# Optimization experiments

Measured on AMD Instinct MI355X. Metric: run time of the kernel, lower is better.

The kernel has to match this reference:

```python
import jax, jax.numpy as jnp
import numpy as np

B = 16384          # batch
F = 64             # number of feature columns (tables)
L = 10             # pooled lookups per feature (bag size)
E = 16             # embedding dim
V = 1_000_000      # hashed vocab size (shared table)
D = F * E          # concat width = 1024
EPS = 1e-5


def setup_inputs() -> dict:
    key = jax.random.key(0)
    ks = jax.random.split(key, 9)
    idx = jax.random.randint(ks[0], (B, F, L), 0, V, dtype=jnp.int64)
    # NormalTensorInitializer(var=0.01) -> std 0.1
    emb = jax.random.normal(ks[1], (V, E), dtype=jnp.float32) * 0.1
    W1 = jax.random.normal(ks[2], (D, 1024), dtype=jnp.float32) / np.sqrt(D).astype(np.float32)
    b1 = jnp.zeros((1024,), jnp.float32)
    W2 = jax.random.normal(ks[3], (1024, 512), dtype=jnp.float32) / np.sqrt(1024).astype(np.float32)
    b2 = jnp.zeros((512,), jnp.float32)
    W3 = jax.random.normal(ks[4], (512, 1), dtype=jnp.float32) / np.sqrt(512).astype(np.float32)
    b3 = jnp.zeros((1,), jnp.float32)
    return {"idx": idx, "emb": emb, "W1": W1, "b1": b1,
            "W2": W2, "b2": b2, "W3": W3, "b3": b3}


def reference(idx, emb, W1, b1, W2, b2, W3, b3):
    # EmbeddingSumConcat: gather [B,F,L,E], sum-pool over bag dim, concat features
    pooled = jnp.take(emb, idx, axis=0).sum(axis=2)          # [B, F, E]
    x = pooled.reshape(B, D)                                  # [B, F*E]
    # ms.nn.Normalization: per-feature batch standardization
    mu = x.mean(axis=0, keepdims=True)
    var = x.var(axis=0, keepdims=True)
    x = (x - mu) * jax.lax.rsqrt(var + EPS)
    # Dense tower 1024 -> 1024 -> 512 -> 1, sigmoid
    h = jax.nn.relu(x @ W1 + b1)
    h = jax.nn.relu(h @ W2 + b2)
    out = jax.nn.sigmoid(h @ W3 + b3)                         # [B, 1]
    return out
```

## Files before the change

### kernel.cpp

```cpp
#include <hip/hip_runtime.h>
#include <hip/hip_bf16.h>
#include <math.h>

typedef __attribute__((ext_vector_type(8))) short  short8;
typedef __attribute__((ext_vector_type(4))) float  f32x4;
typedef __attribute__((ext_vector_type(4))) unsigned short u16x4;
typedef __attribute__((ext_vector_type(8))) unsigned short u16x8;

#define BATCH 16384
#define NF    64
#define BAGL  10
#define ED    16
#define DW    1024
#define VOCAB 1000000

static __device__ __forceinline__ unsigned short f2bf(float f) {
    unsigned int u = __builtin_bit_cast(unsigned int, f);
    unsigned int r = (u + 0x7fffu + ((u >> 16) & 1u)) >> 16;
    return (unsigned short)r;
}
static __device__ __forceinline__ float bf2f(unsigned short h) {
    unsigned int u = ((unsigned int)h) << 16;
    return __builtin_bit_cast(float, u);
}

__global__ __launch_bounds__(256) void pool_kernel(const int* __restrict__ idx,
                                                   const float* __restrict__ emb,
                                                   unsigned short* __restrict__ xb) {
    const int gid = blockIdx.x * 256 + threadIdx.x;
    const int bag = gid >> 2;
    const int q   = gid & 3;
    const int* ip = idx + (long long)bag * BAGL;
    const unsigned qb = (unsigned)(q << 4);

    unsigned o0 = ((unsigned)ip[0] << 6) + qb, o1 = ((unsigned)ip[1] << 6) + qb,
             o2 = ((unsigned)ip[2] << 6) + qb, o3 = ((unsigned)ip[3] << 6) + qb,
             o4 = ((unsigned)ip[4] << 6) + qb, o5 = ((unsigned)ip[5] << 6) + qb,
             o6 = ((unsigned)ip[6] << 6) + qb, o7 = ((unsigned)ip[7] << 6) + qb,
             o8 = ((unsigned)ip[8] << 6) + qb, o9 = ((unsigned)ip[9] << 6) + qb;

    f32x4 e0, e1, e2, e3, e4, e5, e6, e7, e8, e9;
#define GLD(e, o) asm volatile("global_load_dwordx4 %0, %1, %2" \
                               : "=v"(e) : "v"(o), "s"(emb))
    GLD(e0, o0); GLD(e1, o1); GLD(e2, o2); GLD(e3, o3); GLD(e4, o4);
    GLD(e5, o5); GLD(e6, o6); GLD(e7, o7); GLD(e8, o8); GLD(e9, o9);
#undef GLD
    asm volatile("s_waitcnt vmcnt(0)" ::: "memory");
    __builtin_amdgcn_sched_barrier(0);

    f32x4 s01 = e0 + e1, s23 = e2 + e3, s45 = e4 + e5, s67 = e6 + e7, s89 = e8 + e9;
    f32x4 acc = ((s01 + s23) + (s45 + s67)) + s89;

    u16x4 o;
#pragma unroll
    for (int j = 0; j < 4; ++j) o[j] = f2bf(acc[j]);
    *(u16x4*)(xb + (((long long)bag) << 4) + (q << 2)) = o;
}

__global__ __launch_bounds__(256) void stats_kernel(const unsigned short* __restrict__ xb,
                                                    float* __restrict__ ssum,
                                                    float* __restrict__ ssq) {
    const int t = threadIdx.x;
    const long long r0 = (long long)blockIdx.x * 64;
    float s[4] = {0, 0, 0, 0}, q[4] = {0, 0, 0, 0};
    for (int r = 0; r < 64; ++r) {
        const u16x4 v = *(const u16x4*)(xb + (r0 + r) * DW + t * 4);
#pragma unroll
        for (int j = 0; j < 4; ++j) { float f = bf2f(v[j]); s[j] += f; q[j] += f * f; }
    }
#pragma unroll
    for (int j = 0; j < 4; ++j) {
        atomicAdd(&ssum[t * 4 + j], s[j]);
        atomicAdd(&ssq [t * 4 + j], q[j]);
    }
}

static __device__ __forceinline__ float rsig_of(const float* ssum, const float* ssq, int c) {
    const float m = ssum[c] * (1.0f / (float)BATCH);
    const float v = ssq[c] * (1.0f / (float)BATCH) - m * m;
    return rsqrtf(v + 1e-5f);
}

__global__ __launch_bounds__(256) void prep_weights(const float* __restrict__ W1,
                                                    const float* __restrict__ W2,
                                                    const float* __restrict__ ssum,
                                                    const float* __restrict__ ssq,
                                                    unsigned short* __restrict__ w1t,
                                                    unsigned short* __restrict__ w2t) {
    const int z = blockIdx.z;
    const int bx = blockIdx.x, by = blockIdx.y;
    if (z == 1 && bx >= 16) return;
    __shared__ float tile[32][33];
    const int tx = threadIdx.x & 31, ty = threadIdx.x >> 5;
    const float* src = z ? W2 : W1;
    unsigned short* dst = z ? w2t : w1t;
    const int C = z ? 512 : 1024;
#pragma unroll
    for (int i = 0; i < 4; ++i) {
        const int r = by * 32 + ty + i * 8, c = bx * 32 + tx;
        float v = src[(long long)r * C + c];
        if (!z) v *= rsig_of(ssum, ssq, r);
        tile[ty + i * 8][tx] = v;
    }
    __syncthreads();
#pragma unroll
    for (int i = 0; i < 4; ++i) {
        const int oc = bx * 32 + ty + i * 8;
        dst[(long long)oc * 1024 + by * 32 + tx] = f2bf(tile[tx][ty + i * 8]);
    }
}

__global__ __launch_bounds__(256) void b1fold_kernel(const float* __restrict__ W1,
                                                     const float* __restrict__ ssum,
                                                     const float* __restrict__ ssq,
                                                     float* __restrict__ b1n) {
    __shared__ float mu_s[128];
    const int n = blockIdx.x * 256 + threadIdx.x;
    const int k0 = blockIdx.y * 128;
    if (threadIdx.x < 128) {
        const int k = k0 + threadIdx.x;
        mu_s[threadIdx.x] = ssum[k] * (1.0f / (float)BATCH) * rsig_of(ssum, ssq, k);
    }
    __syncthreads();
    float acc = 0.f;
#pragma unroll 4
    for (int k = 0; k < 128; ++k)
        acc += mu_s[k] * W1[(long long)(k0 + k) * 1024 + n];
    atomicAdd(&b1n[n], -acc);
}

__global__ __launch_bounds__(512, 2) void gemm1_256(const unsigned short* __restrict__ A,
                                                    const unsigned short* __restrict__ Bt,
                                                    const float* __restrict__ bias,
                                                    const float* __restrict__ bias2,
                                                    unsigned short* __restrict__ C,
                                                    int M, int N, int K) {
    __shared__ __align__(16) unsigned short As[2][256 * 64];
    __shared__ __align__(16) unsigned short Bs[2][256 * 64];
    const int tid = threadIdx.x;
    const int w = tid >> 6, l = tid & 63;
    const int wr = w >> 2, wc = w & 3;
    const int l15 = l & 15, l4 = l >> 4;
    const int blk = blockIdx.x, xcd = blk & 7, jj = blk >> 3;
    const int bm = xcd * 8 + (jj >> 2), bn = jj & 3;

    f32x4 acc[8][4] = {};
    const long long a_base = (long long)bm * 256 * K;
    const long long b_base = (long long)bn * 256 * K;
    const int NT = K >> 6;

#define G1_STAGE(buf, kt)                                                       \
  {                                                                             \
    const int k0s = (kt) * 64;                                                  \
    _Pragma("unroll")                                                           \
    for (int g = 0; g < 4; ++g) {                                               \
      const int cid = g * 512 + tid;                                            \
      const int rr = cid >> 3, pos = cid & 7;                                   \
      const int csrc = (pos ^ (rr & 7)) << 3;                                   \
      __builtin_amdgcn_global_load_lds(                                         \
        (const __attribute__((address_space(1))) void*)(A + a_base + (long long)rr * K + k0s + csrc), \
        (__attribute__((address_space(3))) void*)(&As[buf][cid * 8]), 16, 0, 0);\
      __builtin_amdgcn_global_load_lds(                                         \
        (const __attribute__((address_space(1))) void*)(Bt + b_base + (long long)rr * K + k0s + csrc), \
        (__attribute__((address_space(3))) void*)(&Bs[buf][cid * 8]), 16, 0, 0);\
    }                                                                           \
  }

    G1_STAGE(0, 0)
    G1_STAGE(1, 1)
    asm volatile("s_waitcnt vmcnt(8)" ::: "memory");
    __builtin_amdgcn_sched_barrier(0);
    __builtin_amdgcn_s_barrier();

    for (int t = 0; t < NT; ++t) {
        const unsigned short* Ap = As[t & 1];
        const unsigned short* Bp = Bs[t & 1];
        short8 a[8], b[4];

        {
            const int swz = (l4 ^ (l15 & 7)) << 3;
#pragma unroll
            for (int m = 0; m < 8; ++m)
                a[m] = *(const short8*)(Ap + (wr * 128 + m * 16 + l15) * 64 + swz);
#pragma unroll
            for (int n = 0; n < 4; ++n)
                b[n] = *(const short8*)(Bp + (wc * 64 + n * 16 + l15) * 64 + swz);
        }
        asm volatile("s_waitcnt lgkmcnt(0)" ::: "memory");
        __builtin_amdgcn_sched_barrier(0);
        __builtin_amdgcn_s_setprio(1);
#pragma unroll
        for (int m = 0; m < 8; ++m)
#pragma unroll
            for (int n = 0; n < 4; ++n)
                acc[m][n] = __builtin_amdgcn_mfma_f32_16x16x32_bf16(a[m], b[n], acc[m][n], 0, 0, 0);
        __builtin_amdgcn_s_setprio(0);

        {
            const int swz = ((4 + l4) ^ (l15 & 7)) << 3;
#pragma unroll
            for (int m = 0; m < 8; ++m)
                a[m] = *(const short8*)(Ap + (wr * 128 + m * 16 + l15) * 64 + swz);
#pragma unroll
            for (int n = 0; n < 4; ++n)
                b[n] = *(const short8*)(Bp + (wc * 64 + n * 16 + l15) * 64 + swz);
        }
        asm volatile("s_waitcnt lgkmcnt(0)" ::: "memory");
        __builtin_amdgcn_sched_barrier(0);
        __builtin_amdgcn_s_barrier();
        if (t + 2 < NT) { G1_STAGE((t & 1), t + 2) }
        __builtin_amdgcn_s_setprio(1);
#pragma unroll
        for (int m = 0; m < 8; ++m)
#pragma unroll
            for (int n = 0; n < 4; ++n)
                acc[m][n] = __builtin_amdgcn_mfma_f32_16x16x32_bf16(a[m], b[n], acc[m][n], 0, 0, 0);
        __builtin_amdgcn_s_setprio(0);
        if (t + 1 < NT) {
            if (t + 2 < NT) { asm volatile("s_waitcnt vmcnt(8)" ::: "memory"); }
            else            { asm volatile("s_waitcnt vmcnt(0)" ::: "memory"); }
            __builtin_amdgcn_sched_barrier(0);
            __builtin_amdgcn_s_barrier();
        }
    }
#undef G1_STAGE

#pragma unroll
    for (int m = 0; m < 8; ++m) {
        const int grow_base = bm * 256 + wr * 128 + m * 16 + l4 * 4;
#pragma unroll
        for (int n = 0; n < 4; ++n) {
            const int gcol = bn * 256 + wc * 64 + n * 16 + l15;
            const float bv = bias[gcol] + bias2[gcol];
#pragma unroll
            for (int j2 = 0; j2 < 4; ++j2) {
                float v = fmaxf(acc[m][n][j2] + bv, 0.f);
                C[(long long)(grow_base + j2) * N + gcol] = f2bf(v);
            }
        }
    }
}

#define GEMM_STAGE(dstA, dstB, kt)                                              \
  {                                                                             \
    const int k0s = (kt) * 64;                                                  \
    _Pragma("unroll")                                                           \
    for (int g = 0; g < 4; ++g) {                                               \
      const int cid = g * 256 + tid;                                            \
      const int rr = cid >> 3, pos = cid & 7;                                   \
      const int csrc = (pos ^ (rr & 7)) << 3;                                   \
      __builtin_amdgcn_global_load_lds(                                         \
        (const __attribute__((address_space(1))) void*)(A + a_base + (long long)rr * K + k0s + csrc), \
        (__attribute__((address_space(3))) void*)(&(dstA)[cid * 8]), 16, 0, 0); \
      __builtin_amdgcn_global_load_lds(                                         \
        (const __attribute__((address_space(1))) void*)(Bt + b_base + (long long)rr * K + k0s + csrc), \
        (__attribute__((address_space(3))) void*)(&(dstB)[cid * 8]), 16, 0, 0); \
    }                                                                           \
  }

__global__ __launch_bounds__(256, 2) void gemm2_fused(const unsigned short* __restrict__ A,
                                                      const unsigned short* __restrict__ Bt,
                                                      const float* __restrict__ bias,
                                                      const float* __restrict__ W3,
                                                      float* __restrict__ logits,
                                                      int M, int N, int K, int NBN) {
    __shared__ __align__(16) unsigned short As[2][128 * 64];
    __shared__ __align__(16) unsigned short Bs[2][128 * 64];
    const int tid = threadIdx.x;
    const int w = tid >> 6, l = tid & 63;
    const int wr = w >> 1, wc = w & 1;
    const int l15 = l & 15, l4 = l >> 4;
    const int blk = blockIdx.x, xcd = blk & 7, j = blk >> 3;
    const int bm = xcd * 16 + j / NBN, bn = j % NBN;

    f32x4 acc[4][4] = {};
    const long long a_base = (long long)bm * 128 * K;
    const long long b_base = (long long)bn * 128 * K;
    const int NT = K >> 6;

    GEMM_STAGE(As[0], Bs[0], 0)
    GEMM_STAGE(As[1], Bs[1], 1)
    asm volatile("s_waitcnt vmcnt(8)" ::: "memory");
    __builtin_amdgcn_sched_barrier(0);
    __builtin_amdgcn_s_barrier();
    for (int t = 0; t < NT; ++t) {
        const unsigned short* Ap = As[t & 1];
        const unsigned short* Bp = Bs[t & 1];
        short8 a[2][4], b[2][4];
#pragma unroll
        for (int kk = 0; kk < 2; ++kk) {
            const int swz = ((kk * 4 + l4) ^ (l15 & 7)) << 3;
#pragma unroll
            for (int m = 0; m < 4; ++m)
                a[kk][m] = *(const short8*)(Ap + (wr * 64 + m * 16 + l15) * 64 + swz);
#pragma unroll
            for (int n = 0; n < 4; ++n)
                b[kk][n] = *(const short8*)(Bp + (wc * 64 + n * 16 + l15) * 64 + swz);
        }
        asm volatile("s_waitcnt lgkmcnt(0)" ::: "memory");
        __builtin_amdgcn_sched_barrier(0);
        __builtin_amdgcn_s_barrier();
        if (t + 2 < NT) { GEMM_STAGE(As[t & 1], Bs[t & 1], t + 2) }
        __builtin_amdgcn_s_setprio(1);
#pragma unroll
        for (int kk = 0; kk < 2; ++kk)
#pragma unroll
            for (int m = 0; m < 4; ++m)
#pragma unroll
                for (int n = 0; n < 4; ++n)
                    acc[m][n] = __builtin_amdgcn_mfma_f32_16x16x32_bf16(a[kk][m], b[kk][n], acc[m][n], 0, 0, 0);
        __builtin_amdgcn_s_setprio(0);
        if (t + 1 < NT) {
            if (t + 2 < NT) { asm volatile("s_waitcnt vmcnt(8)" ::: "memory"); }
            else            { asm volatile("s_waitcnt vmcnt(0)" ::: "memory"); }
            __builtin_amdgcn_sched_barrier(0);
            __builtin_amdgcn_s_barrier();
        }
    }

#pragma unroll
    for (int m = 0; m < 4; ++m) {
        float part[4] = {0.f, 0.f, 0.f, 0.f};
#pragma unroll
        for (int n = 0; n < 4; ++n) {
            const int gcol = bn * 128 + wc * 64 + n * 16 + l15;
            const float bv = bias[gcol];
            const float w3 = W3[gcol];
#pragma unroll
            for (int j2 = 0; j2 < 4; ++j2) {
                float v = fmaxf(acc[m][n][j2] + bv, 0.f);
                part[j2] += v * w3;
            }
        }
#pragma unroll
        for (int off = 1; off < 16; off <<= 1)
#pragma unroll
            for (int j2 = 0; j2 < 4; ++j2) part[j2] += __shfl_xor(part[j2], off, 64);
        if (l15 == 0) {
            const int grow = bm * 128 + wr * 64 + m * 16 + l4 * 4;
#pragma unroll
            for (int j2 = 0; j2 < 4; ++j2) atomicAdd(&logits[grow + j2], part[j2]);
        }
    }
}

__global__ __launch_bounds__(256) void sigmoid_kernel(const float* __restrict__ logits,
                                                      const float* __restrict__ b3,
                                                      float* __restrict__ out) {
    const int i = blockIdx.x * 256 + threadIdx.x;
    out[i] = 1.0f / (1.0f + expf(-(logits[i] + b3[0])));
}

extern "C" void kernel_launch(void* const* d_in, const int* in_sizes, int n_in,
                              void* d_out, int out_size, void* d_ws, size_t ws_size,
                              hipStream_t stream) {
    const int*   idx = (const int*)d_in[0];
    const float* emb = (const float*)d_in[1];
    const float* W1  = (const float*)d_in[2];
    const float* b1  = (const float*)d_in[3];
    const float* W2  = (const float*)d_in[4];
    const float* b2  = (const float*)d_in[5];
    const float* W3  = (const float*)d_in[6];
    const float* b3  = (const float*)d_in[7];
    float* out = (float*)d_out;

    char* ws = (char*)d_ws;
    unsigned short* xb   = (unsigned short*)ws; ws += (size_t)BATCH * DW * 2;
    unsigned short* h1   = (unsigned short*)ws; ws += (size_t)BATCH * DW * 2;
    unsigned short* w1t  = (unsigned short*)ws; ws += (size_t)1024 * 1024 * 2;
    unsigned short* w2t  = (unsigned short*)ws; ws += (size_t)512 * 1024 * 2;
    float* ssum   = (float*)ws; ws += 4096;
    float* ssq    = (float*)ws; ws += 4096;
    float* b1n    = (float*)ws; ws += 4096;
    float* logits = (float*)ws; ws += (size_t)BATCH * 4;

    hipMemsetAsync(ssum, 0, 4096 * 3 + (size_t)BATCH * 4, stream);

    pool_kernel<<<(BATCH * NF * 4) / 256, 256, 0, stream>>>(idx, emb, xb);
    stats_kernel<<<BATCH / 64, 256, 0, stream>>>(xb, ssum, ssq);

    prep_weights<<<dim3(32, 32, 2), 256, 0, stream>>>(W1, W2, ssum, ssq, w1t, w2t);
    b1fold_kernel<<<dim3(4, 8), 256, 0, stream>>>(W1, ssum, ssq, b1n);

    gemm1_256<<<(BATCH / 256) * (1024 / 256), 512, 0, stream>>>(
        xb, w1t, b1, b1n, h1, BATCH, 1024, 1024);
    gemm2_fused<<<(BATCH / 128) * (512 / 128), 256, 0, stream>>>(
        h1, w2t, b2, W3, logits, BATCH, 512, 1024, 512 / 128);

    sigmoid_kernel<<<BATCH / 256, 256, 0, stream>>>(logits, b3, out);
}
```

Baseline: 303.9 us.

## Restructure gemm1 into 8-phase half-tile pipeline and merge small kernels

Rewrites the first GEMM as an 8-phase schedule over half tiles, so each phase loads one quadrant of A/B fragments, issues the next half-tile global-to-LDS load, and runs 16 MFMAs with finer-grained waits. The b1fold kernel is merged into prep_weights as a third z-slice to save a launch. The stats kernel now processes 128 rows per block, halving its atomics. The pooling kernel's inline asm loads are replaced with plain C++ vector loads. The GEMM change aims to overlap memory with MFMA more evenly, but adds barriers per phase.

After: 298.0 us. About the same (-1.9%).

```diff
diff --git a/kernel.cpp b/kernel.cpp
--- a/kernel.cpp
+++ b/kernel.cpp
@@ -31,24 +31,17 @@
     const int bag = gid >> 2;
     const int q   = gid & 3;
     const int* ip = idx + (long long)bag * BAGL;
-    const unsigned qb = (unsigned)(q << 4);
-
-    unsigned o0 = ((unsigned)ip[0] << 6) + qb, o1 = ((unsigned)ip[1] << 6) + qb,
-             o2 = ((unsigned)ip[2] << 6) + qb, o3 = ((unsigned)ip[3] << 6) + qb,
-             o4 = ((unsigned)ip[4] << 6) + qb, o5 = ((unsigned)ip[5] << 6) + qb,
-             o6 = ((unsigned)ip[6] << 6) + qb, o7 = ((unsigned)ip[7] << 6) + qb,
-             o8 = ((unsigned)ip[8] << 6) + qb, o9 = ((unsigned)ip[9] << 6) + qb;
-
-    f32x4 e0, e1, e2, e3, e4, e5, e6, e7, e8, e9;
-#define GLD(e, o) asm volatile("global_load_dwordx4 %0, %1, %2" \
-                               : "=v"(e) : "v"(o), "s"(emb))
-    GLD(e0, o0); GLD(e1, o1); GLD(e2, o2); GLD(e3, o3); GLD(e4, o4);
-    GLD(e5, o5); GLD(e6, o6); GLD(e7, o7); GLD(e8, o8); GLD(e9, o9);
-#undef GLD
-    asm volatile("s_waitcnt vmcnt(0)" ::: "memory");
-    __builtin_amdgcn_sched_barrier(0);
-
-    f32x4 s01 = e0 + e1, s23 = e2 + e3, s45 = e4 + e5, s67 = e6 + e7, s89 = e8 + e9;
+
+    int v[BAGL];
+#pragma unroll
+    for (int l = 0; l < BAGL; ++l) v[l] = ip[l];
+    f32x4 e[BAGL];
+#pragma unroll
+    for (int l = 0; l < BAGL; ++l)
+        e[l] = *(const f32x4*)(emb + (((long long)v[l]) << 4) + (q << 2));
+
+    f32x4 s01 = e[0] + e[1], s23 = e[2] + e[3], s45 = e[4] + e[5],
+          s67 = e[6] + e[7], s89 = e[8] + e[9];
     f32x4 acc = ((s01 + s23) + (s45 + s67)) + s89;
 
     u16x4 o;
@@ -61,9 +54,9 @@
                                                     float* __restrict__ ssum,
                                                     float* __restrict__ ssq) {
     const int t = threadIdx.x;
-    const long long r0 = (long long)blockIdx.x * 64;
+    const long long r0 = (long long)blockIdx.x * 128;
     float s[4] = {0, 0, 0, 0}, q[4] = {0, 0, 0, 0};
-    for (int r = 0; r < 64; ++r) {
+    for (int r = 0; r < 128; ++r) {
         const u16x4 v = *(const u16x4*)(xb + (r0 + r) * DW + t * 4);
 #pragma unroll
         for (int j = 0; j < 4; ++j) { float f = bf2f(v[j]); s[j] += f; q[j] += f * f; }
@@ -86,9 +79,27 @@
                                                     const float* __restrict__ ssum,
                                                     const float* __restrict__ ssq,
                                                     unsigned short* __restrict__ w1t,
-                                                    unsigned short* __restrict__ w2t) {
+                                                    unsigned short* __restrict__ w2t,
+                                                    float* __restrict__ b1n) {
     const int z = blockIdx.z;
     const int bx = blockIdx.x, by = blockIdx.y;
+    if (z == 2) {
+        if (bx >= 4 || by >= 8) return;
+        __shared__ float mu_s[128];
+        const int n = bx * 256 + threadIdx.x;
+        const int k0 = by * 128;
+        if (threadIdx.x < 128) {
+            const int k = k0 + threadIdx.x;
+            mu_s[threadIdx.x] = ssum[k] * (1.0f / (float)BATCH) * rsig_of(ssum, ssq, k);
+        }
+        __syncthreads();
+        float acc = 0.f;
+#pragma unroll 4
+        for (int k = 0; k < 128; ++k)
+            acc += mu_s[k] * W1[(long long)(k0 + k) * 1024 + n];
+        atomicAdd(&b1n[n], -acc);
+        return;
+    }
     if (z == 1 && bx >= 16) return;
     __shared__ float tile[32][33];
     const int tx = threadIdx.x & 31, ty = threadIdx.x >> 5;
@@ -110,131 +121,118 @@
     }
 }
 
-__global__ __launch_bounds__(256) void b1fold_kernel(const float* __restrict__ W1,
-                                                     const float* __restrict__ ssum,
-                                                     const float* __restrict__ ssq,
-                                                     float* __restrict__ b1n) {
-    __shared__ float mu_s[128];
-    const int n = blockIdx.x * 256 + threadIdx.x;
-    const int k0 = blockIdx.y * 128;
-    if (threadIdx.x < 128) {
-        const int k = k0 + threadIdx.x;
-        mu_s[threadIdx.x] = ssum[k] * (1.0f / (float)BATCH) * rsig_of(ssum, ssq, k);
-    }
-    __syncthreads();
-    float acc = 0.f;
-#pragma unroll 4
-    for (int k = 0; k < 128; ++k)
-        acc += mu_s[k] * W1[(long long)(k0 + k) * 1024 + n];
-    atomicAdd(&b1n[n], -acc);
-}
-
-__global__ __launch_bounds__(512, 2) void gemm1_256(const unsigned short* __restrict__ A,
+__global__ __launch_bounds__(512, 2) void gemm1_8ph(const unsigned short* __restrict__ A,
                                                     const unsigned short* __restrict__ Bt,
                                                     const float* __restrict__ bias,
                                                     const float* __restrict__ bias2,
                                                     unsigned short* __restrict__ C,
                                                     int M, int N, int K) {
-    __shared__ __align__(16) unsigned short As[2][256 * 64];
-    __shared__ __align__(16) unsigned short Bs[2][256 * 64];
+    __shared__ __align__(16) unsigned short As[2][2][128 * 64];
+    __shared__ __align__(16) unsigned short Bs[2][2][128 * 64];
     const int tid = threadIdx.x;
     const int w = tid >> 6, l = tid & 63;
-    const int wr = w >> 2, wc = w & 3;
+    const int wr = (w >> 2) & 1, wc = w & 3;
     const int l15 = l & 15, l4 = l >> 4;
     const int blk = blockIdx.x, xcd = blk & 7, jj = blk >> 3;
     const int bm = xcd * 8 + (jj >> 2), bn = jj & 3;
 
     f32x4 acc[8][4] = {};
-    const long long a_base = (long long)bm * 256 * K;
-    const long long b_base = (long long)bn * 256 * K;
-    const int NT = K >> 6;
-
-#define G1_STAGE(buf, kt)                                                       \
+    const int NTILE = K >> 6;
+    const int ITERS = NTILE >> 1;
+    const unsigned short* GA = A  + (long long)bm * 256 * K;
+    const unsigned short* GB = Bt + (long long)bn * 256 * K;
+
+#define ST_HALF(GSRC, LDSN, h, kt)                                              \
+    if ((kt) < NTILE) {                                                         \
+      _Pragma("unroll")                                                         \
+      for (int c = 0; c < 2; ++c) {                                             \
+        const int cid = c * 512 + tid;                                          \
+        const int rr = cid >> 3, pos = cid & 7;                                 \
+        const int csrc = (pos ^ (rr & 7)) << 3;                                 \
+        __builtin_amdgcn_global_load_lds(                                       \
+          (const __attribute__((address_space(1))) void*)(GSRC + ((long long)((h) * 128 + rr)) * K + (kt) * 64 + csrc), \
+          (__attribute__((address_space(3))) void*)(&LDSN[(kt) & 1][h][cid * 8]), 16, 0, 0); \
+      }                                                                         \
+    }
+
+#define PHASE(tt, hm, hn, DOSTAGE, VMN)                                         \
   {                                                                             \
-    const int k0s = (kt) * 64;                                                  \
+    const unsigned short* Ah = &As[(tt) & 1][hm][0];                            \
+    const unsigned short* Bh = &Bs[(tt) & 1][hn][0];                            \
+    short8 af[2][4]; short8 bf[2][2];                                           \
     _Pragma("unroll")                                                           \
-    for (int g = 0; g < 4; ++g) {                                               \
-      const int cid = g * 512 + tid;                                            \
-      const int rr = cid >> 3, pos = cid & 7;                                   \
-      const int csrc = (pos ^ (rr & 7)) << 3;                                   \
-      __builtin_amdgcn_global_load_lds(                                         \
-        (const __attribute__((address_space(1))) void*)(A + a_base + (long long)rr * K + k0s + csrc), \
-        (__attribute__((address_space(3))) void*)(&As[buf][cid * 8]), 16, 0, 0);\
-      __builtin_amdgcn_global_load_lds(                                         \
-        (const __attribute__((address_space(1))) void*)(Bt + b_base + (long long)rr * K + k0s + csrc), \
-        (__attribute__((address_space(3))) void*)(&Bs[buf][cid * 8]), 16, 0, 0);\
+    for (int kk = 0; kk < 2; ++kk) {                                            \
+      const int swz = ((kk * 4 + l4) ^ (l15 & 7)) << 3;                         \
+      _Pragma("unroll")                                                         \
+      for (int m = 0; m < 4; ++m)                                               \
+        af[kk][m] = *(const short8*)(Ah + (wr * 64 + m * 16 + l15) * 64 + swz); \
+      _Pragma("unroll")                                                         \
+      for (int n = 0; n < 2; ++n)                                               \
+        bf[kk][n] = *(const short8*)(Bh + (wc * 32 + n * 16 + l15) * 64 + swz); \
     }                                                                           \
+    DOSTAGE                                                                     \
+    __builtin_amdgcn_s_barrier();                                               \
+    asm volatile("s_waitcnt lgkmcnt(0)" ::: "memory");                          \
+    __builtin_amdgcn_sched_barrier(0);                                          \
+    __builtin_amdgcn_s_setprio(1);                                              \
+    _Pragma("unroll")                                                           \
+    for (int kk = 0; kk < 2; ++kk)                                              \
+      _Pragma("unroll")                                                         \
+      for (int m = 0; m < 4; ++m)                                               \
+        _Pragma("unroll")                                                       \
+        for (int n = 0; n < 2; ++n)                                             \
+          acc[(hm) * 4 + m][(hn) * 2 + n] = __builtin_amdgcn_mfma_f32_16x16x32_bf16( \
+              af[kk][m], bf[kk][n], acc[(hm) * 4 + m][(hn) * 2 + n], 0, 0, 0);  \
+    __builtin_amdgcn_s_setprio(0);                                              \
+    if ((VMN) == 4)      { asm volatile("s_waitcnt vmcnt(4)" ::: "memory"); __builtin_amdgcn_sched_barrier(0); } \
+    else if ((VMN) == 0) { asm volatile("s_waitcnt vmcnt(0)" ::: "memory"); __builtin_amdgcn_sched_barrier(0); } \
+    __builtin_amdgcn_s_barrier();                                               \
   }
 
-    G1_STAGE(0, 0)
-    G1_STAGE(1, 1)
-    asm volatile("s_waitcnt vmcnt(8)" ::: "memory");
+    ST_HALF(GA, As, 0, 0) ST_HALF(GB, Bs, 0, 0)
+    ST_HALF(GA, As, 1, 0) ST_HALF(GB, Bs, 1, 0)
+    ST_HALF(GA, As, 0, 1) ST_HALF(GB, Bs, 0, 1)
+    asm volatile("s_waitcnt vmcnt(4)" ::: "memory");
     __builtin_amdgcn_sched_barrier(0);
     __builtin_amdgcn_s_barrier();
 
-    for (int t = 0; t < NT; ++t) {
-        const unsigned short* Ap = As[t & 1];
-        const unsigned short* Bp = Bs[t & 1];
-        short8 a[8], b[4];
-
-        {
-            const int swz = (l4 ^ (l15 & 7)) << 3;
-#pragma unroll
-            for (int m = 0; m < 8; ++m)
-                a[m] = *(const short8*)(Ap + (wr * 128 + m * 16 + l15) * 64 + swz);
-#pragma unroll
-            for (int n = 0; n < 4; ++n)
-                b[n] = *(const short8*)(Bp + (wc * 64 + n * 16 + l15) * 64 + swz);
-        }
-        asm volatile("s_waitcnt lgkmcnt(0)" ::: "memory");
-        __builtin_amdgcn_sched_barrier(0);
-        __builtin_amdgcn_s_setprio(1);
-#pragma unroll
-        for (int m = 0; m < 8; ++m)
-#pragma unroll
-            for (int n = 0; n < 4; ++n)
-                acc[m][n] = __builtin_amdgcn_mfma_f32_16x16x32_bf16(a[m], b[n], acc[m][n], 0, 0, 0);
-        __builtin_amdgcn_s_setprio(0);
-
-        {
-            const int swz = ((4 + l4) ^ (l15 & 7)) << 3;
-#pragma unroll
-            for (int m = 0; m < 8; ++m)
-                a[m] = *(const short8*)(Ap + (wr * 128 + m * 16 + l15) * 64 + swz);
-#pragma unroll
-            for (int n = 0; n < 4; ++n)
-                b[n] = *(const short8*)(Bp + (wc * 64 + n * 16 + l15) * 64 + swz);
-        }
-        asm volatile("s_waitcnt lgkmcnt(0)" ::: "memory");
-        __builtin_amdgcn_sched_barrier(0);
-        __builtin_amdgcn_s_barrier();
-        if (t + 2 < NT) { G1_STAGE((t & 1), t + 2) }
-        __builtin_amdgcn_s_setprio(1);
-#pragma unroll
-        for (int m = 0; m < 8; ++m)
-#pragma unroll
-            for (int n = 0; n < 4; ++n)
-                acc[m][n] = __builtin_amdgcn_mfma_f32_16x16x32_bf16(a[m], b[n], acc[m][n], 0, 0, 0);
-        __builtin_amdgcn_s_setprio(0);
-        if (t + 1 < NT) {
-            if (t + 2 < NT) { asm volatile("s_waitcnt vmcnt(8)" ::: "memory"); }
-            else            { asm volatile("s_waitcnt vmcnt(0)" ::: "memory"); }
-            __builtin_amdgcn_sched_barrier(0);
-            __builtin_amdgcn_s_barrier();
-        }
-    }
-#undef G1_STAGE
-
-#pragma unroll
-    for (int m = 0; m < 8; ++m) {
-        const int grow_base = bm * 256 + wr * 128 + m * 16 + l4 * 4;
-#pragma unroll
-        for (int n = 0; n < 4; ++n) {
-            const int gcol = bn * 256 + wc * 64 + n * 16 + l15;
+    for (int i = 0; i < ITERS - 1; ++i) {
+        const int t0 = 2 * i, t1 = 2 * i + 1;
+        PHASE(t0, 0, 0, ST_HALF(GA, As, 1, t1),     -1)
+        PHASE(t0, 0, 1, ST_HALF(GB, Bs, 1, t1),     -1)
+        PHASE(t0, 1, 0, ST_HALF(GA, As, 0, t0 + 2), -1)
+        PHASE(t0, 1, 1, ST_HALF(GB, Bs, 0, t0 + 2),  4)
+        PHASE(t1, 0, 0, ST_HALF(GA, As, 1, t0 + 2), -1)
+        PHASE(t1, 0, 1, ST_HALF(GB, Bs, 1, t0 + 2), -1)
+        PHASE(t1, 1, 0, ST_HALF(GA, As, 0, t1 + 2), -1)
+        PHASE(t1, 1, 1, ST_HALF(GB, Bs, 0, t1 + 2),  4)
+    }
+    {
+        const int t0 = NTILE - 2, t1 = NTILE - 1;
+        PHASE(t0, 0, 0, ST_HALF(GA, As, 1, t1), -1)
+        PHASE(t0, 0, 1, ST_HALF(GB, Bs, 1, t1), -1)
+        PHASE(t0, 1, 0, {},                      -1)
+        PHASE(t0, 1, 1, {},                       0)
+        PHASE(t1, 0, 0, {},                      -1)
+        PHASE(t1, 0, 1, {},                      -1)
+        PHASE(t1, 1, 0, {},                      -1)
+        PHASE(t1, 1, 1, {},                      -1)
+    }
+#undef PHASE
+#undef ST_HALF
+
+#pragma unroll
+    for (int mg = 0; mg < 8; ++mg) {
+        const int hm = mg >> 2, m4 = mg & 3;
+        const int grow_base = bm * 256 + hm * 128 + wr * 64 + m4 * 16 + l4 * 4;
+#pragma unroll
+        for (int ng = 0; ng < 4; ++ng) {
+            const int hn = ng >> 1, n4 = ng & 1;
+            const int gcol = bn * 256 + hn * 128 + wc * 32 + n4 * 16 + l15;
             const float bv = bias[gcol] + bias2[gcol];
 #pragma unroll
             for (int j2 = 0; j2 < 4; ++j2) {
-                float v = fmaxf(acc[m][n][j2] + bv, 0.f);
+                float v = fmaxf(acc[mg][ng][j2] + bv, 0.f);
                 C[(long long)(grow_base + j2) * N + gcol] = f2bf(v);
             }
         }
@@ -377,12 +375,11 @@
     hipMemsetAsync(ssum, 0, 4096 * 3 + (size_t)BATCH * 4, stream);
 
     pool_kernel<<<(BATCH * NF * 4) / 256, 256, 0, stream>>>(idx, emb, xb);
-    stats_kernel<<<BATCH / 64, 256, 0, stream>>>(xb, ssum, ssq);
-
-    prep_weights<<<dim3(32, 32, 2), 256, 0, stream>>>(W1, W2, ssum, ssq, w1t, w2t);
-    b1fold_kernel<<<dim3(4, 8), 256, 0, stream>>>(W1, ssum, ssq, b1n);
-
-    gemm1_256<<<(BATCH / 256) * (1024 / 256), 512, 0, stream>>>(
+    stats_kernel<<<BATCH / 128, 256, 0, stream>>>(xb, ssum, ssq);
+
+    prep_weights<<<dim3(32, 32, 3), 256, 0, stream>>>(W1, W2, ssum, ssq, w1t, w2t, b1n);
+
+    gemm1_8ph<<<(BATCH / 256) * (1024 / 256), 512, 0, stream>>>(
         xb, w1t, b1, b1n, h1, BATCH, 1024, 1024);
     gemm2_fused<<<(BATCH / 128) * (512 / 128), 256, 0, stream>>>(
         h1, w2t, b2, W3, logits, BATCH, 512, 1024, 512 / 128);
```
